# Optimization experiments

Measured on AMD Instinct MI355X. Metric: run time of the kernel, lower is better.

The kernel has to match this reference:

```python
import jax, jax.numpy as jnp
import numpy as np

TAU = 0.001
TEMPERATURE = 0.1


def setup_inputs() -> dict:
    key = jax.random.key(0)
    k1, k2 = jax.random.split(key)
    B, H, N, L = 2, 8, 256, 64
    X = jax.random.normal(k1, (B, H, N, L), dtype=jnp.float32)
    Y = jax.random.normal(k2, (B, H, N, L), dtype=jnp.float32)
    return {"X": X, "Y": Y}


def _softsort_p2(scores):
    # scores: [B,H,N,L] -> s: [B,H,L,N]
    s = jnp.transpose(scores, (0, 1, 3, 2))
    srt = -jnp.sort(-s, axis=-1)  # descending sort along N
    # pairwise squared diff: rows = sorted values, cols = original values -> [B,H,L,N,N]
    pd = -((s[..., None, :] - srt[..., :, None]) ** 2) / TAU
    return jax.nn.softmax(pd, axis=-1)


def reference(X, Y):
    # Soft permutation matrices: [B,H,L,N,N]
    Pu = _softsort_p2(X)
    Pv = _softsort_p2(Y)
    # Gamma = Pu^T @ Pv  (contract over sorted-row index i)
    Gamma = jnp.einsum('bhlij,bhlik->bhljk', Pu, Pv)
    # cdist(X, Y, p=2) over last dim L -> [B,H,N,N]
    x2 = jnp.sum(X * X, axis=-1)            # [B,H,N]
    y2 = jnp.sum(Y * Y, axis=-1)            # [B,H,N]
    xy = jnp.einsum('bhnl,bhml->bhnm', X, Y)
    cost = jnp.sqrt(jnp.maximum(x2[..., :, None] + y2[..., None, :] - 2.0 * xy, 1e-12))
    # swds[b,h,l] = sum_{j,k} cost[b,h,j,k] * Gamma[b,h,l,j,k]
    swds = jnp.einsum('bhjk,bhljk->bhl', cost, Gamma)
    # exp(-T*(swds - min)) / sum == softmax(-T * swds) over L
    weights = jax.nn.softmax(-TEMPERATURE * swds, axis=-1)  # [B,H,L]
    # weighted sum over L -> [B,H,N,N]
    return jnp.einsum('bhljk,bhl->bhjk', Gamma, weights)
```

## Files before the change

kernel.cpp:

```cpp
#include <hip/hip_runtime.h>
#include <math.h>

#define INV_TAU 1000.0f
#define TEMP    0.1f
#define CEXP    -1442.6950408889634f
#define SQRTC   37.98283767f


typedef __attribute__((ext_vector_type(8))) _Float16 half8;
typedef __attribute__((ext_vector_type(8))) short short8;
typedef __attribute__((ext_vector_type(4))) float f32x4;
typedef __attribute__((ext_vector_type(2))) float f32x2;
typedef __attribute__((ext_vector_type(2))) unsigned int u32x2;

__device__ __forceinline__ float fexp2(float x) { return __builtin_amdgcn_exp2f(x); }

__device__ __forceinline__ half8 ldsh8(const unsigned short* p) {
  return __builtin_bit_cast(half8, *(const short8*)p);
}

__device__ __forceinline__ unsigned cvt_pk_bf16(float lo, float hi) {
  unsigned r;
  asm("v_cvt_pk_bf16_f32 %0, %1, %2" : "=v"(r) : "v"(lo), "v"(hi));
  return r;
}

__device__ __forceinline__ int tswz(int row, int g) {
  return row * 32 + (((g + (row >> 1)) & 3) << 3);
}

__global__ __launch_bounds__(256) void prep_kernel(const float* __restrict__ X,
                                                   const float* __restrict__ Y,
                                                   float* __restrict__ cost,
                                                   float* __restrict__ nssu, float* __restrict__ lziu,
                                                   float* __restrict__ nssv, float* __restrict__ lziv) {
  __shared__ __align__(16) float smem[256];
  const int tid = threadIdx.x;
  if (blockIdx.x < 1024) {
    const int jq = blockIdx.x & 63, bh = blockIdx.x >> 6;
    const int j0 = jq * 4;
    smem[tid] = X[((size_t)bh*256 + j0 + (tid >> 6))*64 + (tid & 63)];
    __syncthreads();
    const float4* yp = (const float4*)(Y + ((size_t)bh*256 + tid)*64);
    float dot[4] = {0.f,0.f,0.f,0.f}, x2[4] = {0.f,0.f,0.f,0.f}, y2 = 0.f;
#pragma unroll
    for (int t = 0; t < 16; ++t) {
      float4 yv = yp[t];
      y2 += yv.x*yv.x + yv.y*yv.y + yv.z*yv.z + yv.w*yv.w;
#pragma unroll
      for (int r = 0; r < 4; ++r) {
        float4 xv = ((const float4*)(smem + r*64))[t];
        dot[r] += xv.x*yv.x + xv.y*yv.y + xv.z*yv.z + xv.w*yv.w;
        x2[r]  += xv.x*xv.x + xv.y*xv.y + xv.z*xv.z + xv.w*xv.w;
      }
    }
#pragma unroll
    for (int r = 0; r < 4; ++r) {
      float c = x2[r] + y2 - 2.f*dot[r];
      cost[((size_t)bh*256 + j0 + r)*256 + tid] = sqrtf(fmaxf(c, 1e-12f));
    }
  } else {
    const int idx = blockIdx.x - 1024;
    const int l = idx & 63, bh = (idx >> 6) & 15, uv = idx >> 10;
    const float* S = uv ? Y : X;
    float* so = uv ? nssv : nssu;
    float* zo = uv ? lziv : lziu;
    float v = S[((size_t)bh*256 + tid)*64 + l];
#pragma unroll
    for (int k = 2; k <= 256; k <<= 1) {
#pragma unroll
      for (int j = k >> 1; j > 0; j >>= 1) {
        float o;
        if (j >= 64) {
          smem[tid] = v; __syncthreads();
          o = smem[tid ^ j]; __syncthreads();
        } else {
          o = __shfl_xor(v, j, 64);
        }
        const bool up    = ((tid & k) == 0);
        const bool lower = ((tid & j) == 0);
        float mn = fminf(v, o), mx = fmaxf(v, o);
        v = (up == lower) ? mn : mx;
      }
    }
    smem[tid] = v; __syncthreads();
    const int jc = 255 - tid;
    const float sv = smem[jc];
    const int lo = jc > 48 ? jc - 48 : 0;
    const int hi = jc < 207 ? jc + 48 : 255;
    float z = 0.f;
    for (int jj = lo; jj <= hi; ++jj) { float d = smem[jj] - sv; z += fexp2(d*d*CEXP); }
    const int base = (bh*64 + l)*256 + tid;
    so[base] = -SQRTC * sv; zo[base] = -__log2f(z);
  }
}

__device__ __forceinline__ uint4 oct_exp(const float* __restrict__ nss,
                                         const float* __restrict__ lz, float sc) {
  const f32x2 sc2 = {sc, sc};
  f32x2 d0 = sc2 + *(const f32x2*)(nss + 0);
  f32x2 d1 = sc2 + *(const f32x2*)(nss + 2);
  f32x2 d2 = sc2 + *(const f32x2*)(nss + 4);
  f32x2 d3 = sc2 + *(const f32x2*)(nss + 6);
  f32x2 a0 = __builtin_elementwise_fma(-d0, d0, *(const f32x2*)(lz + 0));
  f32x2 a1 = __builtin_elementwise_fma(-d1, d1, *(const f32x2*)(lz + 2));
  f32x2 a2 = __builtin_elementwise_fma(-d2, d2, *(const f32x2*)(lz + 4));
  f32x2 a3 = __builtin_elementwise_fma(-d3, d3, *(const f32x2*)(lz + 6));
  uint4 w;
  w.x = __builtin_bit_cast(unsigned, __builtin_amdgcn_cvt_pkrtz(fexp2(a0.x), fexp2(a0.y)));
  w.y = __builtin_bit_cast(unsigned, __builtin_amdgcn_cvt_pkrtz(fexp2(a1.x), fexp2(a1.y)));
  w.z = __builtin_bit_cast(unsigned, __builtin_amdgcn_cvt_pkrtz(fexp2(a2.x), fexp2(a2.y)));
  w.w = __builtin_bit_cast(unsigned, __builtin_amdgcn_cvt_pkrtz(fexp2(a3.x), fexp2(a3.y)));
  return w;
}

__device__ __forceinline__ void stage_slab(int t, int ib, float usc, float vsc,
                                           const float* __restrict__ nssU, const float* __restrict__ lzU,
                                           const float* __restrict__ nssV, const float* __restrict__ lzV,
                                           unsigned short* __restrict__ EU,
                                           unsigned short* __restrict__ EV) {
  {
    const int r = t & 127, g = t >> 7;
    const int i0 = ib + (g << 3);
    *(uint4*)&EU[tswz(r, g)] = oct_exp(nssU + i0, lzU + i0, usc);
  }
  {
    const int r = t & 255;
    const int gp = (t >> 8) << 1;
#pragma unroll
    for (int gg = 0; gg < 2; ++gg) {
      const int i0 = ib + ((gp + gg) << 3);
      *(uint4*)&EV[tswz(r, gp + gg)] = oct_exp(nssV + i0, lzV + i0, vsc);
    }
  }
}

__global__ __launch_bounds__(512, 4) void pass1_kernel(
    const float* __restrict__ X, const float* __restrict__ Y,
    const float* __restrict__ cost,
    const float* __restrict__ nssu, const float* __restrict__ lziu,
    const float* __restrict__ nssv, const float* __restrict__ lziv,
    float* __restrict__ parts, u32x2* __restrict__ gamma) {
  const int sb = blockIdx.x, l = blockIdx.y, bh = blockIdx.z;
  const int j0 = sb * 128;
  const int tid = threadIdx.x, wave = tid >> 6, lane = tid & 63;
  const int wj = (wave & 1) * 64, wk = (wave >> 1) * 64;
  const int m = lane & 15, q = lane >> 4;
  const int inner = m*32 + (((q + (m >> 1)) & 3) << 3);

  __shared__ __align__(16) float nssU[256], lzU[256], nssV[256], lzV[256];
  __shared__ __align__(16) unsigned short EU0[128*32], EU1[128*32];
  __shared__ __align__(16) unsigned short EV0[256*32], EV1[256*32];
  __shared__ float red[8];

  const int lb = (bh*64 + l)*256;
  const float usc = SQRTC * X[((size_t)bh*256 + j0 + (tid & 127))*64 + l];
  const float vsc = SQRTC * Y[((size_t)bh*256 + (tid & 255))*64 + l];
  if (tid < 256) { nssU[tid] = nssu[lb + tid]; lzU[tid] = lziu[lb + tid]; }
  else { const int t2 = tid - 256; nssV[t2] = nssv[lb + t2]; lzV[t2] = lziv[lb + t2]; }

  f32x4 acc[16];
#pragma unroll
  for (int t = 0; t < 16; ++t) acc[t] = (f32x4){0.f, 0.f, 0.f, 0.f};

  __syncthreads();
  stage_slab(tid, 0, usc, vsc, nssU, lzU, nssV, lzV, EU0, EV0);
  __syncthreads();
#pragma unroll 1
  for (int s = 0; s < 8; ++s) {
    const unsigned short* EUc = (s & 1) ? EU1 : EU0;
    const unsigned short* EVc = (s & 1) ? EV1 : EV0;
    unsigned short* EUn = (s & 1) ? EU0 : EU1;
    unsigned short* EVn = (s & 1) ? EV0 : EV1;
    half8 A[4], B[4];
#pragma unroll
    for (int mt = 0; mt < 4; ++mt) A[mt] = ldsh8(&EUc[(wj + mt*16)*32 + inner]);
#pragma unroll
    for (int nt = 0; nt < 4; ++nt) B[nt] = ldsh8(&EVc[(wk + nt*16)*32 + inner]);
    if (s < 7)
      stage_slab(tid, (s+1)*32, usc, vsc, nssU, lzU, nssV, lzV, EUn, EVn);
#pragma unroll
    for (int mt = 0; mt < 4; ++mt)
#pragma unroll
      for (int nt = 0; nt < 4; ++nt)
        acc[mt*4+nt] = __builtin_amdgcn_mfma_f32_16x16x32_f16(A[mt], B[nt], acc[mt*4+nt], 0, 0, 0);
    __syncthreads();
  }

  const float* cb = cost + (size_t)bh * 65536;
  const int gbase = ((bh*2 + sb)*8 + wave) * 16;
  float part = 0.f;
#pragma unroll
  for (int mt = 0; mt < 4; ++mt) {
#pragma unroll
    for (int nt = 0; nt < 4; ++nt) {
      const int col  = wk + nt*16 + m;
      const int rowb = j0 + wj + mt*16 + q*4;
      f32x4 a = acc[mt*4 + nt];
      part += a.x*cb[(size_t)(rowb+0)*256 + col] + a.y*cb[(size_t)(rowb+1)*256 + col]
            + a.z*cb[(size_t)(rowb+2)*256 + col] + a.w*cb[(size_t)(rowb+3)*256 + col];
      u32x2 pk;
      pk.x = cvt_pk_bf16(a.x, a.y);
      pk.y = cvt_pk_bf16(a.z, a.w);
      __builtin_nontemporal_store(pk, &gamma[((size_t)(gbase + mt*4 + nt)*64 + l)*64 + lane]);
    }
  }
#pragma unroll
  for (int o = 32; o > 0; o >>= 1) part += __shfl_down(part, o, 64);
  if (lane == 0) red[wave] = part;
  __syncthreads();
  if (tid == 0) {
    float s8 = red[0]+red[1]+red[2]+red[3]+red[4]+red[5]+red[6]+red[7];
    parts[sb*1024 + bh*64 + l] = s8;
  }
}

__global__ __launch_bounds__(256) void wsum_kernel(const u32x2* __restrict__ g,
                                                   const float* __restrict__ parts,
                                                   float* __restrict__ out) {
  const int wv = threadIdx.x >> 6, lane = threadIdx.x & 63;
  const int bh = blockIdx.x >> 6;
  __shared__ float w[64];
  if (wv == 0) {
    float s = parts[bh*64 + lane] + parts[1024 + bh*64 + lane];
    float v = -TEMP * s * 1.4426950408889634f;
    float mx = v;
#pragma unroll
    for (int o = 32; o > 0; o >>= 1) mx = fmaxf(mx, __shfl_xor(mx, o, 64));
    float e = fexp2(v - mx);
    float ssum = e;
#pragma unroll
    for (int o = 32; o > 0; o >>= 1) ssum += __shfl_xor(ssum, o, 64);
    w[lane] = e / ssum;
  }
  __syncthreads();
  const int group = blockIdx.x * 4 + wv;
  const u32x2* gp = g + (size_t)group*4096 + lane;
  float4 acc = {0.f, 0.f, 0.f, 0.f};
#pragma unroll 8
  for (int l = 0; l < 64; ++l) {
    u32x2 pk = __builtin_nontemporal_load(gp + l*64);
    float wl = w[l];
    acc.x += wl * __uint_as_float(pk.x << 16);
    acc.y += wl * __uint_as_float(pk.x & 0xFFFF0000u);
    acc.z += wl * __uint_as_float(pk.y << 16);
    acc.w += wl * __uint_as_float(pk.y & 0xFFFF0000u);
  }
  const int frag = group & 15;
  const int idx  = group >> 4;
  const int wave = idx & 7, sbb = (idx >> 3) & 1;
  const int mt = frag >> 2, nt = frag & 3;
  const int m = lane & 15, q = lane >> 4;
  const int row = sbb*128 + (wave & 1)*64 + mt*16 + q*4;
  const int col = (wave >> 1)*64 + nt*16 + m;
  float* ob = out + ((size_t)bh*256 + row)*256 + col;
  __builtin_nontemporal_store(acc.x, &ob[0]);
  __builtin_nontemporal_store(acc.y, &ob[256]);
  __builtin_nontemporal_store(acc.z, &ob[512]);
  __builtin_nontemporal_store(acc.w, &ob[768]);
}

extern "C" void kernel_launch(void* const* d_in, const int* in_sizes, int n_in,
                              void* d_out, int out_size, void* d_ws, size_t ws_size,
                              hipStream_t stream) {
  (void)in_sizes; (void)n_in; (void)out_size; (void)ws_size;
  const float* X = (const float*)d_in[0];
  const float* Y = (const float*)d_in[1];
  float* out = (float*)d_out;
  float* ws  = (float*)d_ws;
  float* cost  = ws;
  float* nssu  = ws   + 1048576;
  float* lziu  = nssu + 262144;
  float* nssv  = lziu + 262144;
  float* lziv  = nssv + 262144;
  float* parts = lziv + 262144;
  u32x2* gamma = (u32x2*)(parts + 2048);

  prep_kernel <<<dim3(3072),      256, 0, stream>>>(X, Y, cost, nssu, lziu, nssv, lziv);
  pass1_kernel<<<dim3(2, 64, 16), 512, 0, stream>>>(X, Y, cost, nssu, lziu, nssv, lziv,
                                                    parts, gamma);
  wsum_kernel <<<dim3(1024),      256, 0, stream>>>(gamma, parts, out);
}
```

Measured before the change: 165.6 us.

## Widen gamma intermediate to 16-byte packs and stagger wsum reads

The bf16 gamma intermediate is now stored and loaded as 128-bit vectors, with each pass1 lane packing two MFMA fragments per store. The reduction kernel uses half as many blocks, each wave handling two fragments. Each wave also starts its L loop at a different offset to spread memory traffic. Separately, the prep kernel's windowed normalizer sum is vectorised to process pairs of elements. That loop now starts at an even index, so it may include one extra element in the sum, which slightly changes the normalizer.

```diff
diff --git a/kernel.cpp b/kernel.cpp
--- a/kernel.cpp
+++ b/kernel.cpp
@@ -11,7 +11,7 @@
 typedef __attribute__((ext_vector_type(8))) short short8;
 typedef __attribute__((ext_vector_type(4))) float f32x4;
 typedef __attribute__((ext_vector_type(2))) float f32x2;
-typedef __attribute__((ext_vector_type(2))) unsigned int u32x2;
+typedef __attribute__((ext_vector_type(4))) unsigned int u32x4;
 
 __device__ __forceinline__ float fexp2(float x) { return __builtin_amdgcn_exp2f(x); }
 
@@ -86,16 +86,25 @@
     smem[tid] = v; __syncthreads();
     const int jc = 255 - tid;
     const float sv = smem[jc];
-    const int lo = jc > 48 ? jc - 48 : 0;
+    int lo = jc > 48 ? jc - 48 : 0;
     const int hi = jc < 207 ? jc + 48 : 255;
-    float z = 0.f;
-    for (int jj = lo; jj <= hi; ++jj) { float d = smem[jj] - sv; z += fexp2(d*d*CEXP); }
+    lo &= ~1;
+    f32x2 z2 = {0.f, 0.f};
+    const f32x2 svv = {sv, sv};
+    const f32x2 cxx = {CEXP, CEXP};
+    for (int p = lo; p <= hi; p += 2) {
+      f32x2 s2 = *(const f32x2*)(smem + p);
+      f32x2 d  = s2 - svv;
+      f32x2 a  = (d * d) * cxx;
+      z2 += (f32x2){fexp2(a.x), fexp2(a.y)};
+    }
+    const float z = z2.x + z2.y;
     const int base = (bh*64 + l)*256 + tid;
     so[base] = -SQRTC * sv; zo[base] = -__log2f(z);
   }
 }
 
-__device__ __forceinline__ uint4 oct_exp(const float* __restrict__ nss,
+__device__ __forceinline__ u32x4 oct_exp(const float* __restrict__ nss,
                                          const float* __restrict__ lz, float sc) {
   const f32x2 sc2 = {sc, sc};
   f32x2 d0 = sc2 + *(const f32x2*)(nss + 0);
@@ -106,11 +115,11 @@
   f32x2 a1 = __builtin_elementwise_fma(-d1, d1, *(const f32x2*)(lz + 2));
   f32x2 a2 = __builtin_elementwise_fma(-d2, d2, *(const f32x2*)(lz + 4));
   f32x2 a3 = __builtin_elementwise_fma(-d3, d3, *(const f32x2*)(lz + 6));
-  uint4 w;
-  w.x = __builtin_bit_cast(unsigned, __builtin_amdgcn_cvt_pkrtz(fexp2(a0.x), fexp2(a0.y)));
-  w.y = __builtin_bit_cast(unsigned, __builtin_amdgcn_cvt_pkrtz(fexp2(a1.x), fexp2(a1.y)));
-  w.z = __builtin_bit_cast(unsigned, __builtin_amdgcn_cvt_pkrtz(fexp2(a2.x), fexp2(a2.y)));
-  w.w = __builtin_bit_cast(unsigned, __builtin_amdgcn_cvt_pkrtz(fexp2(a3.x), fexp2(a3.y)));
+  u32x4 w;
+  w[0] = __builtin_bit_cast(unsigned, __builtin_amdgcn_cvt_pkrtz(fexp2(a0.x), fexp2(a0.y)));
+  w[1] = __builtin_bit_cast(unsigned, __builtin_amdgcn_cvt_pkrtz(fexp2(a1.x), fexp2(a1.y)));
+  w[2] = __builtin_bit_cast(unsigned, __builtin_amdgcn_cvt_pkrtz(fexp2(a2.x), fexp2(a2.y)));
+  w[3] = __builtin_bit_cast(unsigned, __builtin_amdgcn_cvt_pkrtz(fexp2(a3.x), fexp2(a3.y)));
   return w;
 }
 
@@ -122,7 +131,7 @@
   {
     const int r = t & 127, g = t >> 7;
     const int i0 = ib + (g << 3);
-    *(uint4*)&EU[tswz(r, g)] = oct_exp(nssU + i0, lzU + i0, usc);
+    *(u32x4*)&EU[tswz(r, g)] = oct_exp(nssU + i0, lzU + i0, usc);
   }
   {
     const int r = t & 255;
@@ -130,7 +139,7 @@
 #pragma unroll
     for (int gg = 0; gg < 2; ++gg) {
       const int i0 = ib + ((gp + gg) << 3);
-      *(uint4*)&EV[tswz(r, gp + gg)] = oct_exp(nssV + i0, lzV + i0, vsc);
+      *(u32x4*)&EV[tswz(r, gp + gg)] = oct_exp(nssV + i0, lzV + i0, vsc);
     }
   }
 }
@@ -140,7 +149,7 @@
     const float* __restrict__ cost,
     const float* __restrict__ nssu, const float* __restrict__ lziu,
     const float* __restrict__ nssv, const float* __restrict__ lziv,
-    float* __restrict__ parts, u32x2* __restrict__ gamma) {
+    float* __restrict__ parts, u32x4* __restrict__ gamma) {
   const int sb = blockIdx.x, l = blockIdx.y, bh = blockIdx.z;
   const int j0 = sb * 128;
   const int tid = threadIdx.x, wave = tid >> 6, lane = tid & 63;
@@ -188,21 +197,27 @@
   }
 
   const float* cb = cost + (size_t)bh * 65536;
-  const int gbase = ((bh*2 + sb)*8 + wave) * 16;
+  const int c8 = ((bh*2 + sb)*8 + wave) * 8;
   float part = 0.f;
 #pragma unroll
   for (int mt = 0; mt < 4; ++mt) {
 #pragma unroll
-    for (int nt = 0; nt < 4; ++nt) {
-      const int col  = wk + nt*16 + m;
+    for (int nt2 = 0; nt2 < 2; ++nt2) {
+      const int colA = wk + nt2*32 + m;
       const int rowb = j0 + wj + mt*16 + q*4;
-      f32x4 a = acc[mt*4 + nt];
-      part += a.x*cb[(size_t)(rowb+0)*256 + col] + a.y*cb[(size_t)(rowb+1)*256 + col]
-            + a.z*cb[(size_t)(rowb+2)*256 + col] + a.w*cb[(size_t)(rowb+3)*256 + col];
-      u32x2 pk;
-      pk.x = cvt_pk_bf16(a.x, a.y);
-      pk.y = cvt_pk_bf16(a.z, a.w);
-      __builtin_nontemporal_store(pk, &gamma[((size_t)(gbase + mt*4 + nt)*64 + l)*64 + lane]);
+      f32x4 a0 = acc[mt*4 + 2*nt2];
+      f32x4 a1 = acc[mt*4 + 2*nt2 + 1];
+      const float* cr0 = cb + (size_t)rowb*256;
+      part += a0.x*cr0[colA]        + a0.y*cr0[256 + colA]
+            + a0.z*cr0[512 + colA]  + a0.w*cr0[768 + colA]
+            + a1.x*cr0[colA + 16]   + a1.y*cr0[256 + colA + 16]
+            + a1.z*cr0[512 + colA + 16] + a1.w*cr0[768 + colA + 16];
+      u32x4 pk;
+      pk[0] = cvt_pk_bf16(a0.x, a0.y);
+      pk[1] = cvt_pk_bf16(a0.z, a0.w);
+      pk[2] = cvt_pk_bf16(a1.x, a1.y);
+      pk[3] = cvt_pk_bf16(a1.z, a1.w);
+      __builtin_nontemporal_store(pk, &gamma[((size_t)(c8 + mt*2 + nt2)*64 + l)*64 + lane]);
     }
   }
 #pragma unroll
@@ -215,13 +230,14 @@
   }
 }
 
-__global__ __launch_bounds__(256) void wsum_kernel(const u32x2* __restrict__ g,
+__global__ __launch_bounds__(256) void wsum_kernel(const u32x4* __restrict__ g,
                                                    const float* __restrict__ parts,
                                                    float* __restrict__ out) {
   const int wv = threadIdx.x >> 6, lane = threadIdx.x & 63;
-  const int bh = blockIdx.x >> 6;
+  const int c  = blockIdx.x * 4 + wv;
+  const int bh = c >> 7;
   __shared__ float w[64];
-  if (wv == 0) {
+  if (threadIdx.x < 64) {
     float s = parts[bh*64 + lane] + parts[1024 + bh*64 + lane];
     float v = -TEMP * s * 1.4426950408889634f;
     float mx = v;
@@ -234,30 +250,38 @@
     w[lane] = e / ssum;
   }
   __syncthreads();
-  const int group = blockIdx.x * 4 + wv;
-  const u32x2* gp = g + (size_t)group*4096 + lane;
-  float4 acc = {0.f, 0.f, 0.f, 0.f};
-#pragma unroll 8
-  for (int l = 0; l < 64; ++l) {
-    u32x2 pk = __builtin_nontemporal_load(gp + l*64);
+  const u32x4* gp = g + (size_t)c*4096 + lane;
+  const int st = c & 63;
+  float4 accA = {0.f, 0.f, 0.f, 0.f};
+  float4 accB = {0.f, 0.f, 0.f, 0.f};
+#pragma unroll 16
+  for (int p = 0; p < 64; ++p) {
+    const int l = (p + st) & 63;
+    u32x4 pk = __builtin_nontemporal_load(gp + l*64);
     float wl = w[l];
-    acc.x += wl * __uint_as_float(pk.x << 16);
-    acc.y += wl * __uint_as_float(pk.x & 0xFFFF0000u);
-    acc.z += wl * __uint_as_float(pk.y << 16);
-    acc.w += wl * __uint_as_float(pk.y & 0xFFFF0000u);
-  }
-  const int frag = group & 15;
-  const int idx  = group >> 4;
-  const int wave = idx & 7, sbb = (idx >> 3) & 1;
-  const int mt = frag >> 2, nt = frag & 3;
+    accA.x += wl * __uint_as_float(pk[0] << 16);
+    accA.y += wl * __uint_as_float(pk[0] & 0xFFFF0000u);
+    accA.z += wl * __uint_as_float(pk[1] << 16);
+    accA.w += wl * __uint_as_float(pk[1] & 0xFFFF0000u);
+    accB.x += wl * __uint_as_float(pk[2] << 16);
+    accB.y += wl * __uint_as_float(pk[2] & 0xFFFF0000u);
+    accB.z += wl * __uint_as_float(pk[3] << 16);
+    accB.w += wl * __uint_as_float(pk[3] & 0xFFFF0000u);
+  }
+  const int nt2 = c & 1, mt = (c >> 1) & 3, rest = c >> 3;
+  const int wave = rest & 7, sbb = (rest >> 3) & 1;
   const int m = lane & 15, q = lane >> 4;
-  const int row = sbb*128 + (wave & 1)*64 + mt*16 + q*4;
-  const int col = (wave >> 1)*64 + nt*16 + m;
-  float* ob = out + ((size_t)bh*256 + row)*256 + col;
-  __builtin_nontemporal_store(acc.x, &ob[0]);
-  __builtin_nontemporal_store(acc.y, &ob[256]);
-  __builtin_nontemporal_store(acc.z, &ob[512]);
-  __builtin_nontemporal_store(acc.w, &ob[768]);
+  const int row  = sbb*128 + (wave & 1)*64 + mt*16 + q*4;
+  const int colA = (wave >> 1)*64 + nt2*32 + m;
+  float* ob = out + ((size_t)bh*256 + row)*256 + colA;
+  __builtin_nontemporal_store(accA.x, &ob[0]);
+  __builtin_nontemporal_store(accA.y, &ob[256]);
+  __builtin_nontemporal_store(accA.z, &ob[512]);
+  __builtin_nontemporal_store(accA.w, &ob[768]);
+  __builtin_nontemporal_store(accB.x, &ob[16]);
+  __builtin_nontemporal_store(accB.y, &ob[272]);
+  __builtin_nontemporal_store(accB.z, &ob[528]);
+  __builtin_nontemporal_store(accB.w, &ob[784]);
 }
 
 extern "C" void kernel_launch(void* const* d_in, const int* in_sizes, int n_in,
@@ -274,10 +298,10 @@
   float* nssv  = lziu + 262144;
   float* lziv  = nssv + 262144;
   float* parts = lziv + 262144;
-  u32x2* gamma = (u32x2*)(parts + 2048);
+  u32x4* gamma = (u32x4*)(parts + 2048);
 
   prep_kernel <<<dim3(3072),      256, 0, stream>>>(X, Y, cost, nssu, lziu, nssv, lziv);
   pass1_kernel<<<dim3(2, 64, 16), 512, 0, stream>>>(X, Y, cost, nssu, lziu, nssv, lziv,
                                                     parts, gamma);
-  wsum_kernel <<<dim3(1024),      256, 0, stream>>>(gamma, parts, out);
-}
+  wsum_kernel <<<dim3(512),       256, 0, stream>>>(gamma, parts, out);
+}
```

Measured after the change: 166.1 us. No clear change (+0.3%).
